# Kernel optimization log

Measured on AMD Instinct MI355X. Metric: run time of the kernel, lower is better.

The kernel has to match this reference:

```python
import jax, jax.numpy as jnp
import numpy as np

B, S, HID = 1, 2048, 3584
NUM_HEADS, KV_HEADS, HEAD_DIM = 28, 4, 128
MROPE = [16, 24, 24]
HEAVY_RATIO, RECENT_RATIO, SINK, MIN_SEQ = 0.1, 0.1, 4, 1024
SCALING = HEAD_DIM ** -0.5
ROPE_THETA = 1000000.0


def rotate_half(x):
    h = x.shape[-1] // 2
    return jnp.concatenate([-x[..., h:], x[..., :h]], axis=-1)


def apply_mrope(q, k, cos, sin, mrope_section):
    # cos/sin: [3, B, S, head_dim]; interleave sections from the 3 position axes
    sec = mrope_section * 2
    splits = list(np.cumsum(sec)[:-1])
    cos_m = jnp.concatenate([m[i % 3] for i, m in enumerate(jnp.split(cos, splits, axis=-1))], axis=-1)[:, None]  # [B,1,S,D]
    sin_m = jnp.concatenate([m[i % 3] for i, m in enumerate(jnp.split(sin, splits, axis=-1))], axis=-1)[:, None]
    q_emb = q * cos_m + rotate_half(q) * sin_m
    k_emb = k * cos_m + rotate_half(k) * sin_m
    return q_emb, k_emb


def h2o_keep_mask(attn_weights, kv_len):
    # attn_weights: [B, H, Q, KV] post-softmax; accumulated score per head/key
    scores = attn_weights.sum(axis=(0, 2))  # [H, KV]
    heavy = max(1, int(HEAVY_RATIO * kv_len))
    recent = max(1, int(RECENT_RATIO * kv_len))
    keep = jnp.zeros((NUM_HEADS, kv_len), dtype=bool)
    ips = max(SINK * 2, int(0.2 * kv_len))  # image-protect prefix
    if kv_len > 3 * ips:
        keep = keep.at[:, :ips].set(True)
        ms = ips
    else:
        keep = keep.at[:, :SINK].set(True)
        ms = SINK
    keep = keep.at[:, kv_len - recent:].set(True)
    me = kv_len - recent
    k = min(heavy, me - ms)
    _, idx = jax.lax.top_k(scores[:, ms:me], k)  # [H, k]
    keep = keep.at[jnp.arange(NUM_HEADS)[:, None], idx + ms].set(True)
    return keep[None, :, None, :]  # [1, H, 1, KV]


def setup_inputs() -> dict:
    key = jax.random.key(0)
    ks = jax.random.split(key, 8)
    hidden_states = jax.random.normal(ks[0], (B, S, HID), jnp.float32)
    # additive causal mask
    causal = jnp.triu(jnp.full((S, S), -1e9, jnp.float32), k=1)
    attention_mask = causal[None, None]
    # mrope cos/sin (same positions on all 3 axes for text-only prefill)
    inv_freq = 1.0 / (ROPE_THETA ** (jnp.arange(0, HEAD_DIM, 2, dtype=jnp.float32) / HEAD_DIM))
    pos = jnp.arange(S, dtype=jnp.float32)
    freqs = pos[:, None] * inv_freq[None, :]            # [S, D/2]
    emb = jnp.concatenate([freqs, freqs], axis=-1)      # [S, D]
    cos = jnp.broadcast_to(jnp.cos(emb)[None, None], (3, B, S, HEAD_DIM))
    sin = jnp.broadcast_to(jnp.sin(emb)[None, None], (3, B, S, HEAD_DIM))
    sd = 0.02
    q_w = jax.random.normal(ks[1], (NUM_HEADS * HEAD_DIM, HID), jnp.float32) * sd
    q_b = jax.random.normal(ks[2], (NUM_HEADS * HEAD_DIM,), jnp.float32) * sd
    k_w = jax.random.normal(ks[3], (KV_HEADS * HEAD_DIM, HID), jnp.float32) * sd
    k_b = jax.random.normal(ks[4], (KV_HEADS * HEAD_DIM,), jnp.float32) * sd
    v_w = jax.random.normal(ks[5], (KV_HEADS * HEAD_DIM, HID), jnp.float32) * sd
    v_b = jax.random.normal(ks[6], (KV_HEADS * HEAD_DIM,), jnp.float32) * sd
    o_w = jax.random.normal(ks[7], (HID, NUM_HEADS * HEAD_DIM), jnp.float32) * sd
    return {"hidden_states": hidden_states, "attention_mask": attention_mask, "cos": cos, "sin": sin,
            "q_w": q_w, "q_b": q_b, "k_w": k_w, "k_b": k_b, "v_w": v_w, "v_b": v_b, "o_w": o_w}


def reference(hidden_states, attention_mask, cos, sin, q_w, q_b, k_w, k_b, v_w, v_b, o_w):
    b, s, _ = hidden_states.shape
    q = (hidden_states @ q_w.T + q_b).reshape(b, s, NUM_HEADS, HEAD_DIM).transpose(0, 2, 1, 3)
    k = (hidden_states @ k_w.T + k_b).reshape(b, s, KV_HEADS, HEAD_DIM).transpose(0, 2, 1, 3)
    v = (hidden_states @ v_w.T + v_b).reshape(b, s, KV_HEADS, HEAD_DIM).transpose(0, 2, 1, 3)
    q, k = apply_mrope(q, k, cos, sin, MROPE)
    n_rep = NUM_HEADS // KV_HEADS
    k = jnp.repeat(k, n_rep, axis=1)  # matches torch repeat_kv layout
    v = jnp.repeat(v, n_rep, axis=1)
    aw = jnp.einsum('bhqd,bhkd->bhqk', q, k) * SCALING + attention_mask
    aw = jax.nn.softmax(aw.astype(jnp.float32), axis=-1).astype(q.dtype)
    kv_len = s
    heavy = max(1, int(HEAVY_RATIO * kv_len))
    recent = max(1, int(RECENT_RATIO * kv_len))
    if kv_len >= MIN_SEQ and kv_len > SINK + recent + heavy:
        mask = h2o_keep_mask(jax.lax.stop_gradient(aw), kv_len)
        aw = aw * mask.astype(aw.dtype)
        aw = aw / jnp.clip(aw.sum(-1, keepdims=True), 1e-9)
    out = jnp.einsum('bhqk,bhkd->bhqd', aw, v)
    out = out.transpose(0, 2, 1, 3).reshape(b, s, NUM_HEADS * HEAD_DIM)
    return out @ o_w.T
```

## Files before the change

### kernel.cpp

```cpp
#include <hip/hip_runtime.h>
#include <hip/hip_bf16.h>
#include <stdint.h>

#define S_LEN 2048
#define HID 3584
#define NHEADS 28
#define KVHEADS 4
#define HD 128
#define QKV_N 4608
#define NREP 7
#define SCALE 0.08838834764831845f
#define NJOBS 896
#define NJOBS_KC 1120

typedef __attribute__((ext_vector_type(8))) short bf16x8;
typedef __attribute__((ext_vector_type(8))) _Float16 f16x8;
typedef __attribute__((ext_vector_type(4))) float f32x4;

#define MFMA_B16(a, b, c) __builtin_amdgcn_mfma_f32_16x16x32_bf16((a), (b), (c), 0, 0, 0)
#define MFMA_F16(a, b, c) __builtin_amdgcn_mfma_f32_16x16x32_f16((a), (b), (c), 0, 0, 0)

__device__ __forceinline__ void gl_lds16(const void* g, void* l) {
  __builtin_amdgcn_global_load_lds(
      (__attribute__((address_space(1))) void*)(void*)(g),
      (__attribute__((address_space(3))) void*)(l), 16, 0, 0);
}

__device__ __forceinline__ void decode_qc(int t, int& qb, int& ck) {
  if (t < 4) { qb = t; ck = 0; }
  else if (t < 12) { qb = 4 + ((t - 4) >> 1); ck = (t - 4) & 1; }
  else if (t < 24) { qb = 8 + (t - 12) / 3; ck = (t - 12) % 3; }
  else { qb = 12 + ((t - 24) >> 2); ck = (t - 24) & 3; }
}

__global__ void cvt_f32_f16(const float* __restrict__ src, _Float16* __restrict__ dst, int n4) {
  int i = blockIdx.x * 256 + threadIdx.x;
  if (i >= n4) return;
  float4 v = ((const float4*)src)[i];
  _Float16 t[4] = {(_Float16)v.x, (_Float16)v.y, (_Float16)v.z, (_Float16)v.w};
  ((uint2*)dst)[i] = *(const uint2*)t;
}

template <bool HAS_BIAS>
__global__ __launch_bounds__(256, 4) void gemm_f16(
    const _Float16* __restrict__ A, int lda,
    const _Float16* __restrict__ B, int ldb,
    const float* __restrict__ bias, float* __restrict__ C, int ldc, int K) {
  __shared__ _Float16 lA[128 * 64], lB[128 * 64];
  const int tid = threadIdx.x;
  const int lane = tid & 63;
  const int wid = tid >> 6;
  const int wr = wid >> 1, wc = wid & 1;
  const int l15 = lane & 15, l4 = lane >> 4;
  const int bm = blockIdx.y * 128, bn = blockIdx.x * 128;
  f32x4 acc[4][4] = {};
  for (int k0 = 0; k0 < K; k0 += 64) {
    __syncthreads();
#pragma unroll
    for (int it = 0; it < 4; ++it) {
      int c = it * 256 + tid;
      int rw = c >> 3, sl = c & 7;
      int gcol = (sl ^ (rw & 7)) << 3;
      int lo = (it * 256 + (tid & 192)) * 8;
      gl_lds16(A + (size_t)(bm + rw) * lda + (k0 + gcol), &lA[lo]);
      gl_lds16(B + (size_t)(bn + rw) * ldb + (k0 + gcol), &lB[lo]);
    }
    __syncthreads();
#pragma unroll
    for (int kk = 0; kk < 2; ++kk) {
      f16x8 af[4], bf[4];
#pragma unroll
      for (int m = 0; m < 4; ++m) {
        int rA = wr * 64 + m * 16 + l15;
        af[m] = *(const f16x8*)&lA[rA * 64 + (((kk * 4 + l4) ^ (rA & 7)) << 3)];
      }
#pragma unroll
      for (int n = 0; n < 4; ++n) {
        int rB = wc * 64 + n * 16 + l15;
        bf[n] = *(const f16x8*)&lB[rB * 64 + (((kk * 4 + l4) ^ (rB & 7)) << 3)];
      }
#pragma unroll
      for (int m = 0; m < 4; ++m)
#pragma unroll
        for (int n = 0; n < 4; ++n)
          acc[m][n] = MFMA_F16(af[m], bf[n], acc[m][n]);
    }
  }
#pragma unroll
  for (int m = 0; m < 4; ++m)
#pragma unroll
    for (int n = 0; n < 4; ++n)
#pragma unroll
      for (int r = 0; r < 4; ++r) {
        size_t row = bm + wr * 64 + m * 16 + l4 * 4 + r;
        size_t col = bn + wc * 64 + n * 16 + l15;
        float v = acc[m][n][r];
        if (HAS_BIAS) v += bias[col];
        C[row * ldc + col] = v;
      }
}

__global__ void rope_f16(const float* __restrict__ qf, const float* __restrict__ cb,
                         const float* __restrict__ sb,
                         _Float16* __restrict__ q16, _Float16* __restrict__ k16) {
  int idx = blockIdx.x * 256 + threadIdx.x;
  int d1 = idx & 63;
  int hh = (idx >> 6) & 31;
  int s = idx >> 11;
  if (s >= S_LEN) return;
  const float* row = qf + (size_t)s * QKV_N + (hh < NHEADS ? hh * HD : HID + (hh - NHEADS) * HD);
  int d2 = d1 + 64;
  int ax1 = (d1 < 32) ? 0 : 1;
  int ax2 = (d2 < 80) ? 1 : 2;
  float c1 = cb[(size_t)ax1 * S_LEN * HD + (size_t)s * HD + d1];
  float s1 = sb[(size_t)ax1 * S_LEN * HD + (size_t)s * HD + d1];
  float c2 = cb[(size_t)ax2 * S_LEN * HD + (size_t)s * HD + d2];
  float s2 = sb[(size_t)ax2 * S_LEN * HD + (size_t)s * HD + d2];
  float x1 = row[d1], x2 = row[d2];
  float y1 = x1 * c1 - x2 * s1;
  float y2 = x2 * c2 + x1 * s2;
  _Float16* dp;
  size_t base;
  if (hh < NHEADS) { dp = q16; base = (size_t)s * HID + hh * HD; }
  else { dp = k16; base = (size_t)s * 512 + (hh - NHEADS) * HD; }
  dp[base + d1] = (_Float16)y1;
  dp[base + d2] = (_Float16)y2;
}

__global__ void vtrans(const float* __restrict__ qf, __hip_bfloat16* __restrict__ vt) {
  __shared__ __hip_bfloat16 t[64][65];
  const int j = blockIdx.z;
  const int d0 = blockIdx.y * 64;
  const int k0 = blockIdx.x * 64;
  const int tid = threadIdx.x;
#pragma unroll
  for (int half = 0; half < 2; ++half) {
    int r = half * 32 + (tid >> 3);
    int c = (tid & 7) * 8;
    const float* p = qf + (size_t)(k0 + r) * QKV_N + (HID + 512) + j * HD + d0 + c;
    float4 a = ((const float4*)p)[0];
    float4 b = ((const float4*)p)[1];
    t[c + 0][r] = __float2bfloat16(a.x); t[c + 1][r] = __float2bfloat16(a.y);
    t[c + 2][r] = __float2bfloat16(a.z); t[c + 3][r] = __float2bfloat16(a.w);
    t[c + 4][r] = __float2bfloat16(b.x); t[c + 5][r] = __float2bfloat16(b.y);
    t[c + 6][r] = __float2bfloat16(b.z); t[c + 7][r] = __float2bfloat16(b.w);
  }
  __syncthreads();
#pragma unroll
  for (int half = 0; half < 2; ++half) {
    int r = half * 32 + (tid >> 3);
    int c = (tid & 7) * 8;
    __hip_bfloat16 tmp[8];
#pragma unroll
    for (int u = 0; u < 8; ++u) tmp[u] = t[r][c + u];
    *(bf16x8*)&vt[(size_t)j * (HD * S_LEN) + (size_t)(d0 + r) * S_LEN + k0 + c] = *(const bf16x8*)tmp;
  }
}

template <typename T>
__device__ __forceinline__ void stageK_sw(T* dst, const T* gsrc, int ldg, int tid) {
#pragma unroll
  for (int it = 0; it < 4; ++it) {
    int c = it * 256 + tid;
    int rw = c >> 4, sl = c & 15;
    int gcol = (sl ^ (rw & 7)) << 3;
    gl_lds16(gsrc + (size_t)rw * ldg + gcol, dst + (size_t)(it * 256 + (tid & 192)) * 8);
  }
}
__device__ __forceinline__ void stageV_sw(__hip_bfloat16* dst, const __hip_bfloat16* gsrc,
                                          int ldg, int tid) {
#pragma unroll
  for (int it = 0; it < 4; ++it) {
    int c = it * 256 + tid;
    int rw = c >> 3, sl = c & 7;
    int gcol = (sl ^ (rw & 7)) << 3;
    gl_lds16(gsrc + (size_t)rw * ldg + gcol, dst + (size_t)(it * 256 + (tid & 192)) * 8);
  }
}

__global__ __launch_bounds__(256, 4) void attn_l(
    const _Float16* __restrict__ q16, const _Float16* __restrict__ k16,
    float* __restrict__ lbuf) {
  __shared__ _Float16 Kh[2][64 * 128];
  const int j = blockIdx.x;
  const int h = j % 28;
  int qb, ck;
  decode_qc(j / 28, qb, ck);
  const int hkv = h / NREP;
  const int nt = 2 * qb + 2;
  const int kt0 = ck * 8;
  const int kt1 = (kt0 + 8 < nt) ? kt0 + 8 : nt;
  const int tid = threadIdx.x;
  const int lane = tid & 63, w = tid >> 6;
  const int l15 = lane & 15, l4 = lane >> 4;
  const int sw = l15 & 7;
  f16x8 qh[2][4];
#pragma unroll
  for (int f = 0; f < 2; ++f) {
    const _Float16* qp =
        q16 + (size_t)(qb * 128 + w * 32 + f * 16 + l15) * HID + h * HD + l4 * 8;
#pragma unroll
    for (int kk = 0; kk < 4; ++kk) qh[f][kk] = *(const f16x8*)(qp + kk * 32);
  }
  float lsum[2][4] = {};
  stageK_sw(Kh[0], k16 + (size_t)(kt0 * 64) * 512 + hkv * HD, 512, tid);
  __syncthreads();
  for (int kt = kt0; kt < kt1; ++kt) {
    if (kt + 1 < kt1)
      stageK_sw(Kh[(kt + 1) & 1], k16 + (size_t)((kt + 1) * 64) * 512 + hkv * HD, 512, tid);
    const _Float16* Kc = Kh[kt & 1];
    f32x4 acc[2][4] = {};
#pragma unroll
    for (int kk = 0; kk < 4; ++kk)
#pragma unroll
      for (int n = 0; n < 4; ++n) {
        f16x8 bh = *(const f16x8*)&Kc[(n * 16 + l15) * 128 + (((kk * 4 + l4) ^ sw) << 3)];
#pragma unroll
        for (int f = 0; f < 2; ++f) acc[f][n] = MFMA_F16(qh[f][kk], bh, acc[f][n]);
      }
    if (kt < 2 * qb) {
#pragma unroll
      for (int f = 0; f < 2; ++f)
#pragma unroll
        for (int r = 0; r < 4; ++r)
#pragma unroll
          for (int n = 0; n < 4; ++n)
            lsum[f][r] += __expf(acc[f][n][r] * SCALE);
    } else {
#pragma unroll
      for (int f = 0; f < 2; ++f)
#pragma unroll
        for (int r = 0; r < 4; ++r) {
          int rowg = qb * 128 + w * 32 + f * 16 + l4 * 4 + r;
#pragma unroll
          for (int n = 0; n < 4; ++n)
            if ((kt * 64 + n * 16 + l15) <= rowg)
              lsum[f][r] += __expf(acc[f][n][r] * SCALE);
        }
    }
    __syncthreads();
  }
#pragma unroll
  for (int f = 0; f < 2; ++f)
#pragma unroll
    for (int r = 0; r < 4; ++r) {
      float s = lsum[f][r];
      s += __shfl_xor(s, 1);
      s += __shfl_xor(s, 2);
      s += __shfl_xor(s, 4);
      s += __shfl_xor(s, 8);
      if (l15 == 0)
        atomicAdd(&lbuf[h * S_LEN + qb * 128 + w * 32 + f * 16 + l4 * 4 + r], s);
    }
}

__global__ __launch_bounds__(256, 4) void attn_sc(
    const _Float16* __restrict__ q16, const _Float16* __restrict__ k16,
    const float* __restrict__ lbuf, float* __restrict__ scores) {
  __shared__ _Float16 Kh[2][64 * 128];
  const int j = blockIdx.x;
  const int h = j % 28;
  int qb, ck;
  decode_qc(j / 28, qb, ck);
  const int hkv = h / NREP;
  const int nt = 2 * qb + 2;
  const int kt0 = ck * 8;
  const int kt1 = (kt0 + 8 < nt) ? kt0 + 8 : nt;
  const int tid = threadIdx.x;
  const int lane = tid & 63, w = tid >> 6;
  const int l15 = lane & 15, l4 = lane >> 4;
  const int sw = l15 & 7;
  f16x8 qh[2][4];
#pragma unroll
  for (int f = 0; f < 2; ++f) {
    const _Float16* qp =
        q16 + (size_t)(qb * 128 + w * 32 + f * 16 + l15) * HID + h * HD + l4 * 8;
#pragma unroll
    for (int kk = 0; kk < 4; ++kk) qh[f][kk] = *(const f16x8*)(qp + kk * 32);
  }
  float invl[2][4];
#pragma unroll
  for (int f = 0; f < 2; ++f)
#pragma unroll
    for (int r = 0; r < 4; ++r)
      invl[f][r] = 1.0f / lbuf[h * S_LEN + qb * 128 + w * 32 + f * 16 + l4 * 4 + r];
  stageK_sw(Kh[0], k16 + (size_t)(kt0 * 64) * 512 + hkv * HD, 512, tid);
  __syncthreads();
  for (int kt = kt0; kt < kt1; ++kt) {
    if (kt + 1 < kt1)
      stageK_sw(Kh[(kt + 1) & 1], k16 + (size_t)((kt + 1) * 64) * 512 + hkv * HD, 512, tid);
    const _Float16* Kc = Kh[kt & 1];
    f32x4 acc[2][4] = {};
#pragma unroll
    for (int kk = 0; kk < 4; ++kk)
#pragma unroll
      for (int n = 0; n < 4; ++n) {
        f16x8 bh = *(const f16x8*)&Kc[(n * 16 + l15) * 128 + (((kk * 4 + l4) ^ sw) << 3)];
#pragma unroll
        for (int f = 0; f < 2; ++f) acc[f][n] = MFMA_F16(qh[f][kk], bh, acc[f][n]);
      }
    float colsum[4] = {0.f, 0.f, 0.f, 0.f};
    if (kt < 2 * qb) {
#pragma unroll
      for (int f = 0; f < 2; ++f)
#pragma unroll
        for (int r = 0; r < 4; ++r)
#pragma unroll
          for (int n = 0; n < 4; ++n)
            colsum[n] += __expf(acc[f][n][r] * SCALE) * invl[f][r];
    } else {
#pragma unroll
      for (int f = 0; f < 2; ++f)
#pragma unroll
        for (int r = 0; r < 4; ++r) {
          int rowg = qb * 128 + w * 32 + f * 16 + l4 * 4 + r;
#pragma unroll
          for (int n = 0; n < 4; ++n)
            if ((kt * 64 + n * 16 + l15) <= rowg)
              colsum[n] += __expf(acc[f][n][r] * SCALE) * invl[f][r];
        }
    }
#pragma unroll
    for (int n = 0; n < 4; ++n) {
      colsum[n] += __shfl_xor(colsum[n], 16);
      colsum[n] += __shfl_xor(colsum[n], 32);
    }
    if (lane < 16) {
#pragma unroll
      for (int n = 0; n < 4; ++n)
        atomicAdd(&scores[h * S_LEN + kt * 64 + n * 16 + lane], colsum[n]);
    }
    __syncthreads();
  }
}

__global__ void h2o_topk(const float* __restrict__ scores, unsigned char* __restrict__ keep) {
  const int h = blockIdx.x;
  const int tid = threadIdx.x;
  const int MS = 409, ME = 1844, REGN = 1435, KSEL = 204;
  __shared__ float sv[1435];
  __shared__ int cnt, eqn;
  __shared__ int eqlist[256];
  for (int i = tid; i < REGN; i += 256) sv[i] = scores[h * S_LEN + MS + i];
  for (int i = tid; i < S_LEN; i += 256)
    keep[h * S_LEN + i] = (i < MS || i >= ME) ? 1 : 0;
  __syncthreads();
  unsigned lo = 0u, hi = 0x7f800000u;
  while (hi - lo > 1u) {
    unsigned mid = lo + ((hi - lo) >> 1);
    if (tid == 0) cnt = 0;
    __syncthreads();
    int lc = 0;
    for (int i = tid; i < REGN; i += 256) lc += (__float_as_uint(sv[i]) >= mid) ? 1 : 0;
    if (lc) atomicAdd(&cnt, lc);
    __syncthreads();
    int c = cnt;
    __syncthreads();
    if (c >= KSEL) lo = mid;
    else hi = mid;
  }
  if (tid == 0) { cnt = 0; eqn = 0; }
  __syncthreads();
  int lgt = 0;
  for (int i = tid; i < REGN; i += 256) {
    unsigned b = __float_as_uint(sv[i]);
    if (b > lo) { keep[h * S_LEN + MS + i] = 1; lgt++; }
    else if (b == lo) {
      int p = atomicAdd(&eqn, 1);
      if (p < 256) eqlist[p] = i;
    }
  }
  if (lgt) atomicAdd(&cnt, lgt);
  __syncthreads();
  if (tid == 0) {
    int r = KSEL - cnt;
    int ne = eqn > 256 ? 256 : eqn;
    for (int t = 0; t < r; ++t) {
      int best = 0x7fffffff, bj = -1;
      for (int j = 0; j < ne; ++j)
        if (eqlist[j] < best) { best = eqlist[j]; bj = j; }
      if (bj < 0) break;
      keep[h * S_LEN + MS + best] = 1;
      eqlist[bj] = 0x7fffffff;
    }
  }
}

__global__ __launch_bounds__(256, 2) void attn_out(
    const _Float16* __restrict__ q16, const _Float16* __restrict__ k16,
    const __hip_bfloat16* __restrict__ vt, const unsigned char* __restrict__ keep,
    _Float16* __restrict__ ctx, int* __restrict__ ctr) {
  __shared__ _Float16 Kh[2][64 * 128];
  __shared__ __hip_bfloat16 Vtl[2][128 * 64];
  __shared__ __hip_bfloat16 Wt[4][16 * 64];
  __shared__ int sj;
  const int tid = threadIdx.x;
  const int lane = tid & 63, w = tid >> 6;
  const int l15 = lane & 15, l4 = lane >> 4;
  const int sw = l15 & 7;
  for (;;) {
    __syncthreads();
    if (tid == 0) sj = atomicAdd(ctr, 1);
    __syncthreads();
    const int j = sj;
    if (j >= NJOBS) return;
    const int qb = 31 - j / 28, h = j % 28;
    const int hkv = h / NREP;
    const int nt = qb + 1;
    f16x8 qh[4];
    {
      const _Float16* qp = q16 + (size_t)(qb * 64 + w * 16 + l15) * HID + h * HD + l4 * 8;
#pragma unroll
      for (int kk = 0; kk < 4; ++kk) qh[kk] = *(const f16x8*)(qp + kk * 32);
    }
    f32x4 o[8] = {};
    float dens[4] = {0.f, 0.f, 0.f, 0.f};
    stageK_sw(Kh[0], k16 + hkv * HD, 512, tid);
    stageV_sw(Vtl[0], vt + (size_t)hkv * (HD * S_LEN), S_LEN, tid);
    __syncthreads();
    for (int kt = 0; kt < nt; ++kt) {
      if (kt + 1 < nt) {
        stageK_sw(Kh[(kt + 1) & 1], k16 + (size_t)((kt + 1) * 64) * 512 + hkv * HD, 512, tid);
        stageV_sw(Vtl[(kt + 1) & 1], vt + (size_t)hkv * (HD * S_LEN) + (kt + 1) * 64, S_LEN, tid);
      }
      const _Float16* Kc = Kh[kt & 1];
      const __hip_bfloat16* Vc = Vtl[kt & 1];
      f32x4 acc[4] = {};
#pragma unroll
      for (int kk = 0; kk < 4; ++kk)
#pragma unroll
        for (int n = 0; n < 4; ++n) {
          f16x8 bh = *(const f16x8*)&Kc[(n * 16 + l15) * 128 + (((kk * 4 + l4) ^ sw) << 3)];
          acc[n] = MFMA_F16(qh[kk], bh, acc[n]);
        }
      const bool diag = (kt == qb);
      float kf[4];
#pragma unroll
      for (int n = 0; n < 4; ++n)
        kf[n] = (float)keep[h * S_LEN + kt * 64 + n * 16 + l15];
#pragma unroll
      for (int r = 0; r < 4; ++r) {
        int rowg = qb * 64 + w * 16 + l4 * 4 + r;
        int row16 = l4 * 4 + r;
#pragma unroll
        for (int n = 0; n < 4; ++n) {
          int coll = n * 16 + l15;
          float wv = 0.f;
          if (!diag || (kt * 64 + coll) <= rowg)
            wv = kf[n] * __expf(acc[n][r] * SCALE);
          dens[r] += wv;
          Wt[w][row16 * 64 + (coll ^ ((row16 & 7) << 3))] = __float2bfloat16(wv);
        }
      }
#pragma unroll
      for (int kk = 0; kk < 2; ++kk) {
        bf16x8 af = *(const bf16x8*)&Wt[w][l15 * 64 + ((kk * 32 + l4 * 8) ^ (sw << 3))];
#pragma unroll
        for (int n = 0; n < 8; ++n) {
          bf16x8 bf = *(const bf16x8*)&Vc[(n * 16 + l15) * 64 + (((kk * 4 + l4) ^ sw) << 3)];
          o[n] = MFMA_B16(af, bf, o[n]);
        }
      }
      __syncthreads();
    }
    float invd[4];
#pragma unroll
    for (int r = 0; r < 4; ++r) {
      float d = dens[r];
      d += __shfl_xor(d, 1);
      d += __shfl_xor(d, 2);
      d += __shfl_xor(d, 4);
      d += __shfl_xor(d, 8);
      invd[r] = 1.0f / fmaxf(d, 1e-30f);
    }
#pragma unroll
    for (int n = 0; n < 8; ++n)
#pragma unroll
      for (int r = 0; r < 4; ++r) {
        size_t row = qb * 64 + w * 16 + l4 * 4 + r;
        size_t col = h * HD + n * 16 + l15;
        ctx[row * HID + col] = (_Float16)(o[n][r] * invd[r]);
      }
  }
}

extern "C" void kernel_launch(void* const* d_in, const int* in_sizes, int n_in,
                              void* d_out, int out_size, void* d_ws, size_t ws_size,
                              hipStream_t stream) {
  const float* hidden = (const float*)d_in[0];
  const float* cosb = (const float*)d_in[2];
  const float* sinb = (const float*)d_in[3];
  const float* q_w = (const float*)d_in[4];
  const float* q_b = (const float*)d_in[5];
  const float* k_w = (const float*)d_in[6];
  const float* k_b = (const float*)d_in[7];
  const float* v_w = (const float*)d_in[8];
  const float* v_b = (const float*)d_in[9];
  const float* o_w = (const float*)d_in[10];

  char* ws = (char*)d_ws;
  float* qkv_f32 = (float*)(ws + 0);
  _Float16* hf16 = (_Float16*)(ws + 37748736);
  _Float16* wqkv16 = (_Float16*)(ws + 52428800);
  float* biasb = (float*)(ws + 85458944);
  _Float16* q16 = (_Float16*)(ws + 37748736);
  _Float16* wo16 = (_Float16*)(ws + 52428800);
  _Float16* k16 = (_Float16*)(ws + 85477376);
  __hip_bfloat16* vt = (__hip_bfloat16*)(ws + 87574528);
  float* scores = (float*)(ws + 89671680);
  unsigned char* keep = (unsigned char*)(ws + 89901056);
  int* ctrs = (int*)(ws + 89958400);
  float* lbuf = (float*)(ws + 89958464);
  _Float16* ctx16 = (_Float16*)(ws + 0);

  hipMemcpyAsync(biasb, q_b, 3584 * 4, hipMemcpyDeviceToDevice, stream);
  hipMemcpyAsync(biasb + 3584, k_b, 512 * 4, hipMemcpyDeviceToDevice, stream);
  hipMemcpyAsync(biasb + 4096, v_b, 512 * 4, hipMemcpyDeviceToDevice, stream);

  cvt_f32_f16<<<7168, 256, 0, stream>>>(hidden, hf16, 1835008);
  cvt_f32_f16<<<12544, 256, 0, stream>>>(q_w, wqkv16, 3211264);
  cvt_f32_f16<<<1792, 256, 0, stream>>>(k_w, wqkv16 + (size_t)3584 * 3584, 458752);
  cvt_f32_f16<<<1792, 256, 0, stream>>>(v_w, wqkv16 + (size_t)4096 * 3584, 458752);

  gemm_f16<true><<<dim3(36, 16), 256, 0, stream>>>(hf16, HID, wqkv16, HID,
                                                   biasb, qkv_f32, QKV_N, HID);

  cvt_f32_f16<<<12544, 256, 0, stream>>>(o_w, wo16, 3211264);

  rope_f16<<<16384, 256, 0, stream>>>(qkv_f32, cosb, sinb, q16, k16);
  vtrans<<<dim3(32, 2, 4), 256, 0, stream>>>(qkv_f32, vt);
  hipMemsetAsync(scores, 0, NHEADS * S_LEN * 4, stream);
  hipMemsetAsync(lbuf, 0, NHEADS * S_LEN * 4, stream);
  hipMemsetAsync(ctrs, 0, 64, stream);

  attn_l<<<NJOBS_KC, 256, 0, stream>>>(q16, k16, lbuf);
  attn_sc<<<NJOBS_KC, 256, 0, stream>>>(q16, k16, lbuf, scores);
  h2o_topk<<<28, 256, 0, stream>>>(scores, keep);
  attn_out<<<512, 256, 0, stream>>>(q16, k16, vt, keep, ctx16, &ctrs[1]);

  gemm_f16<false><<<dim3(28, 16), 256, 0, stream>>>(ctx16, HID, wo16, HID,
                                                    nullptr, (float*)d_out, HID, HID);
}
```

Before: 420.5 us.

## Split attention output over key chunks with atomic accumulation and separate normalization

Replaces the persistent atomic-counter attention-output kernel with a static grid of 1120 jobs. Each job covers 128 query rows and up to 8 key tiles, so long causal rows are split across blocks. Partial outputs and denominators are accumulated with float atomics into an fp32 buffer, and a new ctx_norm kernel then normalizes and converts to fp16. This is meant to even out load imbalance and raise parallelism, at the cost of a 29MB memset, atomic traffic and an extra pass. It also merges the three q/k/v weight conversion launches into one.

```diff
diff --git a/kernel.cpp b/kernel.cpp
--- a/kernel.cpp
+++ b/kernel.cpp
@@ -10,7 +10,6 @@
 #define QKV_N 4608
 #define NREP 7
 #define SCALE 0.08838834764831845f
-#define NJOBS 896
 #define NJOBS_KC 1120
 
 typedef __attribute__((ext_vector_type(8))) short bf16x8;
@@ -37,6 +36,20 @@
   int i = blockIdx.x * 256 + threadIdx.x;
   if (i >= n4) return;
   float4 v = ((const float4*)src)[i];
+  _Float16 t[4] = {(_Float16)v.x, (_Float16)v.y, (_Float16)v.z, (_Float16)v.w};
+  ((uint2*)dst)[i] = *(const uint2*)t;
+}
+
+__global__ void cvt_qkvw(const float* __restrict__ qw, const float* __restrict__ kw,
+                         const float* __restrict__ vw, _Float16* __restrict__ dst) {
+  int i = blockIdx.x * 256 + threadIdx.x;
+  if (i >= 4128768) return;
+  const float* src;
+  int off;
+  if (i < 3211264) { src = qw; off = i; }
+  else if (i < 3670016) { src = kw; off = i - 3211264; }
+  else { src = vw; off = i - 3670016; }
+  float4 v = ((const float4*)src)[off];
   _Float16 t[4] = {(_Float16)v.x, (_Float16)v.y, (_Float16)v.z, (_Float16)v.w};
   ((uint2*)dst)[i] = *(const uint2*)t;
 }
@@ -386,102 +399,128 @@
   }
 }
 
-__global__ __launch_bounds__(256, 2) void attn_out(
+__global__ __launch_bounds__(256, 2) void attn_oc(
     const _Float16* __restrict__ q16, const _Float16* __restrict__ k16,
     const __hip_bfloat16* __restrict__ vt, const unsigned char* __restrict__ keep,
-    _Float16* __restrict__ ctx, int* __restrict__ ctr) {
+    float* __restrict__ ctxf, float* __restrict__ densb) {
   __shared__ _Float16 Kh[2][64 * 128];
   __shared__ __hip_bfloat16 Vtl[2][128 * 64];
-  __shared__ __hip_bfloat16 Wt[4][16 * 64];
-  __shared__ int sj;
+  __shared__ __hip_bfloat16 Wt[4][32 * 64];
+  const int j = blockIdx.x;
+  const int h = j % 28;
+  int qb, ck;
+  decode_qc(39 - j / 28, qb, ck);
+  const int hkv = h / NREP;
+  const int nt = 2 * qb + 2;
+  const int kt0 = ck * 8;
+  const int kt1 = (kt0 + 8 < nt) ? kt0 + 8 : nt;
   const int tid = threadIdx.x;
   const int lane = tid & 63, w = tid >> 6;
   const int l15 = lane & 15, l4 = lane >> 4;
   const int sw = l15 & 7;
-  for (;;) {
-    __syncthreads();
-    if (tid == 0) sj = atomicAdd(ctr, 1);
-    __syncthreads();
-    const int j = sj;
-    if (j >= NJOBS) return;
-    const int qb = 31 - j / 28, h = j % 28;
-    const int hkv = h / NREP;
-    const int nt = qb + 1;
-    f16x8 qh[4];
-    {
-      const _Float16* qp = q16 + (size_t)(qb * 64 + w * 16 + l15) * HID + h * HD + l4 * 8;
-#pragma unroll
-      for (int kk = 0; kk < 4; ++kk) qh[kk] = *(const f16x8*)(qp + kk * 32);
-    }
-    f32x4 o[8] = {};
-    float dens[4] = {0.f, 0.f, 0.f, 0.f};
-    stageK_sw(Kh[0], k16 + hkv * HD, 512, tid);
-    stageV_sw(Vtl[0], vt + (size_t)hkv * (HD * S_LEN), S_LEN, tid);
-    __syncthreads();
-    for (int kt = 0; kt < nt; ++kt) {
-      if (kt + 1 < nt) {
-        stageK_sw(Kh[(kt + 1) & 1], k16 + (size_t)((kt + 1) * 64) * 512 + hkv * HD, 512, tid);
-        stageV_sw(Vtl[(kt + 1) & 1], vt + (size_t)hkv * (HD * S_LEN) + (kt + 1) * 64, S_LEN, tid);
-      }
-      const _Float16* Kc = Kh[kt & 1];
-      const __hip_bfloat16* Vc = Vtl[kt & 1];
-      f32x4 acc[4] = {};
-#pragma unroll
-      for (int kk = 0; kk < 4; ++kk)
-#pragma unroll
-        for (int n = 0; n < 4; ++n) {
-          f16x8 bh = *(const f16x8*)&Kc[(n * 16 + l15) * 128 + (((kk * 4 + l4) ^ sw) << 3)];
-          acc[n] = MFMA_F16(qh[kk], bh, acc[n]);
-        }
-      const bool diag = (kt == qb);
-      float kf[4];
-#pragma unroll
-      for (int n = 0; n < 4; ++n)
-        kf[n] = (float)keep[h * S_LEN + kt * 64 + n * 16 + l15];
+  f16x8 qh[2][4];
+#pragma unroll
+  for (int f = 0; f < 2; ++f) {
+    const _Float16* qp =
+        q16 + (size_t)(qb * 128 + w * 32 + f * 16 + l15) * HID + h * HD + l4 * 8;
+#pragma unroll
+    for (int kk = 0; kk < 4; ++kk) qh[f][kk] = *(const f16x8*)(qp + kk * 32);
+  }
+  f32x4 o[2][8] = {};
+  float dens[2][4] = {};
+  stageK_sw(Kh[0], k16 + (size_t)(kt0 * 64) * 512 + hkv * HD, 512, tid);
+  stageV_sw(Vtl[0], vt + (size_t)hkv * (HD * S_LEN) + kt0 * 64, S_LEN, tid);
+  __syncthreads();
+  for (int kt = kt0; kt < kt1; ++kt) {
+    if (kt + 1 < kt1) {
+      stageK_sw(Kh[(kt + 1) & 1], k16 + (size_t)((kt + 1) * 64) * 512 + hkv * HD, 512, tid);
+      stageV_sw(Vtl[(kt + 1) & 1], vt + (size_t)hkv * (HD * S_LEN) + (kt + 1) * 64, S_LEN, tid);
+    }
+    const _Float16* Kc = Kh[kt & 1];
+    const __hip_bfloat16* Vc = Vtl[kt & 1];
+    f32x4 acc[2][4] = {};
+#pragma unroll
+    for (int kk = 0; kk < 4; ++kk)
+#pragma unroll
+      for (int n = 0; n < 4; ++n) {
+        f16x8 bh = *(const f16x8*)&Kc[(n * 16 + l15) * 128 + (((kk * 4 + l4) ^ sw) << 3)];
+#pragma unroll
+        for (int f = 0; f < 2; ++f) acc[f][n] = MFMA_F16(qh[f][kk], bh, acc[f][n]);
+      }
+    float kf[4];
+#pragma unroll
+    for (int n = 0; n < 4; ++n)
+      kf[n] = (float)keep[h * S_LEN + kt * 64 + n * 16 + l15];
+    const bool tail = (kt >= 2 * qb);
+#pragma unroll
+    for (int f = 0; f < 2; ++f)
 #pragma unroll
       for (int r = 0; r < 4; ++r) {
-        int rowg = qb * 64 + w * 16 + l4 * 4 + r;
-        int row16 = l4 * 4 + r;
+        int rowg = qb * 128 + w * 32 + f * 16 + l4 * 4 + r;
+        int row32 = f * 16 + l4 * 4 + r;
 #pragma unroll
         for (int n = 0; n < 4; ++n) {
           int coll = n * 16 + l15;
           float wv = 0.f;
-          if (!diag || (kt * 64 + coll) <= rowg)
-            wv = kf[n] * __expf(acc[n][r] * SCALE);
-          dens[r] += wv;
-          Wt[w][row16 * 64 + (coll ^ ((row16 & 7) << 3))] = __float2bfloat16(wv);
+          if (!tail || (kt * 64 + coll) <= rowg)
+            wv = kf[n] * __expf(acc[f][n][r] * SCALE);
+          dens[f][r] += wv;
+          Wt[w][row32 * 64 + (coll ^ ((row32 & 7) << 3))] = __float2bfloat16(wv);
         }
       }
 #pragma unroll
-      for (int kk = 0; kk < 2; ++kk) {
-        bf16x8 af = *(const bf16x8*)&Wt[w][l15 * 64 + ((kk * 32 + l4 * 8) ^ (sw << 3))];
-#pragma unroll
-        for (int n = 0; n < 8; ++n) {
-          bf16x8 bf = *(const bf16x8*)&Vc[(n * 16 + l15) * 64 + (((kk * 4 + l4) ^ sw) << 3)];
-          o[n] = MFMA_B16(af, bf, o[n]);
-        }
-      }
-      __syncthreads();
-    }
-    float invd[4];
+    for (int kk = 0; kk < 2; ++kk) {
+      bf16x8 af[2];
+#pragma unroll
+      for (int f = 0; f < 2; ++f) {
+        int rowW = f * 16 + l15;
+        af[f] = *(const bf16x8*)&Wt[w][rowW * 64 + ((kk * 32 + l4 * 8) ^ ((rowW & 7) << 3))];
+      }
+#pragma unroll
+      for (int n = 0; n < 8; ++n) {
+        bf16x8 bf = *(const bf16x8*)&Vc[(n * 16 + l15) * 64 + (((kk * 4 + l4) ^ sw) << 3)];
+#pragma unroll
+        for (int f = 0; f < 2; ++f) o[f][n] = MFMA_B16(af[f], bf, o[f][n]);
+      }
+    }
+    __syncthreads();
+  }
+#pragma unroll
+  for (int f = 0; f < 2; ++f)
 #pragma unroll
     for (int r = 0; r < 4; ++r) {
-      float d = dens[r];
+      float d = dens[f][r];
       d += __shfl_xor(d, 1);
       d += __shfl_xor(d, 2);
       d += __shfl_xor(d, 4);
       d += __shfl_xor(d, 8);
-      invd[r] = 1.0f / fmaxf(d, 1e-30f);
-    }
+      if (l15 == 0)
+        atomicAdd(&densb[h * S_LEN + qb * 128 + w * 32 + f * 16 + l4 * 4 + r], d);
+    }
+#pragma unroll
+  for (int f = 0; f < 2; ++f)
 #pragma unroll
     for (int n = 0; n < 8; ++n)
 #pragma unroll
       for (int r = 0; r < 4; ++r) {
-        size_t row = qb * 64 + w * 16 + l4 * 4 + r;
+        size_t row = qb * 128 + w * 32 + f * 16 + l4 * 4 + r;
         size_t col = h * HD + n * 16 + l15;
-        ctx[row * HID + col] = (_Float16)(o[n][r] * invd[r]);
-      }
-  }
+        atomicAdd(&ctxf[row * HID + col], o[f][n][r]);
+      }
+}
+
+__global__ void ctx_norm(const float* __restrict__ cf, const float* __restrict__ densb,
+                         _Float16* __restrict__ out) {
+  int i = blockIdx.x * 256 + threadIdx.x;
+  if (i >= 1835008) return;
+  int col4 = i % (HID / 4);
+  int row = i / (HID / 4);
+  int h = (col4 * 4) / HD;
+  float inv = 1.0f / fmaxf(densb[h * S_LEN + row], 1e-30f);
+  float4 v = ((const float4*)cf)[i];
+  _Float16 t[4] = {(_Float16)(v.x * inv), (_Float16)(v.y * inv),
+                   (_Float16)(v.z * inv), (_Float16)(v.w * inv)};
+  ((uint2*)out)[i] = *(const uint2*)t;
 }
 
 extern "C" void kernel_launch(void* const* d_in, const int* in_sizes, int n_in,
@@ -509,18 +548,17 @@
   __hip_bfloat16* vt = (__hip_bfloat16*)(ws + 87574528);
   float* scores = (float*)(ws + 89671680);
   unsigned char* keep = (unsigned char*)(ws + 89901056);
-  int* ctrs = (int*)(ws + 89958400);
   float* lbuf = (float*)(ws + 89958464);
-  _Float16* ctx16 = (_Float16*)(ws + 0);
+  float* densb = (float*)(ws + 90187840);
+  float* ctx_f32 = (float*)(ws + 0);
+  _Float16* ctx16 = (_Float16*)(ws + 37748736);
 
   hipMemcpyAsync(biasb, q_b, 3584 * 4, hipMemcpyDeviceToDevice, stream);
   hipMemcpyAsync(biasb + 3584, k_b, 512 * 4, hipMemcpyDeviceToDevice, stream);
   hipMemcpyAsync(biasb + 4096, v_b, 512 * 4, hipMemcpyDeviceToDevice, stream);
 
   cvt_f32_f16<<<7168, 256, 0, stream>>>(hidden, hf16, 1835008);
-  cvt_f32_f16<<<12544, 256, 0, stream>>>(q_w, wqkv16, 3211264);
-  cvt_f32_f16<<<1792, 256, 0, stream>>>(k_w, wqkv16 + (size_t)3584 * 3584, 458752);
-  cvt_f32_f16<<<1792, 256, 0, stream>>>(v_w, wqkv16 + (size_t)4096 * 3584, 458752);
+  cvt_qkvw<<<16128, 256, 0, stream>>>(q_w, k_w, v_w, wqkv16);
 
   gemm_f16<true><<<dim3(36, 16), 256, 0, stream>>>(hf16, HID, wqkv16, HID,
                                                    biasb, qkv_f32, QKV_N, HID);
@@ -529,14 +567,16 @@
 
   rope_f16<<<16384, 256, 0, stream>>>(qkv_f32, cosb, sinb, q16, k16);
   vtrans<<<dim3(32, 2, 4), 256, 0, stream>>>(qkv_f32, vt);
+  hipMemsetAsync(ctx_f32, 0, 29360128, stream);
   hipMemsetAsync(scores, 0, NHEADS * S_LEN * 4, stream);
   hipMemsetAsync(lbuf, 0, NHEADS * S_LEN * 4, stream);
-  hipMemsetAsync(ctrs, 0, 64, stream);
+  hipMemsetAsync(densb, 0, NHEADS * S_LEN * 4, stream);
 
   attn_l<<<NJOBS_KC, 256, 0, stream>>>(q16, k16, lbuf);
   attn_sc<<<NJOBS_KC, 256, 0, stream>>>(q16, k16, lbuf, scores);
   h2o_topk<<<28, 256, 0, stream>>>(scores, keep);
-  attn_out<<<512, 256, 0, stream>>>(q16, k16, vt, keep, ctx16, &ctrs[1]);
+  attn_oc<<<NJOBS_KC, 256, 0, stream>>>(q16, k16, vt, keep, ctx_f32, densb);
+  ctx_norm<<<7168, 256, 0, stream>>>(ctx_f32, densb, ctx16);
 
   gemm_f16<false><<<dim3(28, 16), 256, 0, stream>>>(ctx16, HID, wo16, HID,
                                                     nullptr, (float*)d_out, HID, HID);
```

After: 460.3 us. 1.09x slower.
